# Performance work log

Measured on AMD Instinct MI355X. Metric: run time of the kernel, lower is better.

The kernel has to match this reference:

```python
import jax, jax.numpy as jnp
import numpy as np

EPS = 1e-5

def _layernorm(x, w, b):
    mu = jnp.mean(x, axis=-1, keepdims=True)
    var = jnp.var(x, axis=-1, keepdims=True)
    return (x - mu) * jax.lax.rsqrt(var + EPS) * w + b

def setup_inputs() -> dict:
    key = jax.random.key(0)
    ks = jax.random.split(key, 7)
    b, n, m, d, h = 4, 1024, 1024, 1024, 16
    sc = 1.0 / np.sqrt(d)
    return {
        "x": jax.random.normal(ks[0], (b, n, d), jnp.float32),
        "xa": jax.random.normal(ks[1], (b, m, d), jnp.float32),
        "ln_w": jnp.ones((d,), jnp.float32),
        "ln_b": jnp.zeros((d,), jnp.float32),
        "Wq": jax.random.normal(ks[2], (d, d), jnp.float32) * sc,
        "Wkv": jax.random.normal(ks[3], (d, 2 * d), jnp.float32) * sc,
        "Wout": jax.random.normal(ks[4], (d, d), jnp.float32) * sc,
    }

def reference(x, xa, ln_w, ln_b, Wq, Wkv, Wout):
    b, n, d = x.shape
    m = xa.shape[1]
    h = 16
    hd = d // h

    xn = _layernorm(x, ln_w, ln_b)
    xan = _layernorm(xa, ln_w, ln_b)

    q = xn @ Wq                      # [b,n,d]
    kv = xn @ Wkv                    # [b,n,2d] (k,v unused for x->xa path except v)
    k, v = kv[..., :d], kv[..., d:]
    kva = xan @ Wkv
    ka, va = kva[..., :d], kva[..., d:]

    split = lambda t: t.reshape(t.shape[0], t.shape[1], h, hd).transpose(0, 2, 1, 3)  # [b,h,s,hd]
    q, v, ka, va = map(split, (q, v, ka, va))

    # shared score matrix: scores[b,h,n,m] = q . ka  (no scaling in source)
    scores = jnp.einsum('bhnd,bhmd->bhnm', q, ka)
    # x -> attends over xa: softmax over m
    probs_x = jax.nn.softmax(scores, axis=-1)
    x_upd = jnp.einsum('bhnm,bhmd->bhnd', probs_x, va)
    # xa -> attends over x: softmax over n (of transposed scores)
    probs_xa = jax.nn.softmax(scores.transpose(0, 1, 3, 2), axis=-1)  # [b,h,m,n]
    xa_upd = jnp.einsum('bhmn,bhnd->bhmd', probs_xa, v)

    merge = lambda t: t.transpose(0, 2, 1, 3).reshape(t.shape[0], t.shape[2], d)
    return (merge(x_upd) @ Wout, merge(xa_upd) @ Wout)
```

## Files before the change

### kernel.cpp

```cpp
#include <hip/hip_runtime.h>
#include <hip/hip_bf16.h>

typedef unsigned short u16;
typedef unsigned int u32;
typedef __attribute__((ext_vector_type(4))) unsigned short u16x4;
typedef __attribute__((ext_vector_type(8))) unsigned short u16x8;
typedef __attribute__((ext_vector_type(8))) __bf16 bf16x8;
typedef __attribute__((ext_vector_type(4))) float f32x4;

__device__ __forceinline__ u16 f2bf(float f){
  unsigned u = __builtin_bit_cast(unsigned, f);
  u += 0x7FFFu + ((u >> 16) & 1u);
  return (u16)(u >> 16);
}

__device__ __forceinline__ u32 cvtpk(float lo, float hi){
  u32 r;
  asm("v_cvt_pk_bf16_f32 %0, %1, %2" : "=v"(r) : "v"(lo), "v"(hi));
  return r;
}

__device__ __forceinline__ void load_lds16(const void* g, void* l){
  __builtin_amdgcn_global_load_lds((const __attribute__((address_space(1))) unsigned*)g,
                                   (__attribute__((address_space(3))) unsigned*)l, 16, 0, 0);
}

__device__ __forceinline__ void storeC(float* p, float v){ *p = v; }
__device__ __forceinline__ void storeC(u16* p, float v){ *p = f2bf(v); }

__global__ __launch_bounds__(256) void transpose_all(const float* __restrict__ Wq,
                                                     const float* __restrict__ Wkv,
                                                     const float* __restrict__ Wout,
                                                     u16* __restrict__ WqT, u16* __restrict__ WkT,
                                                     u16* __restrict__ WvT, u16* __restrict__ WoT){
  const float* in; u16* out; int ldin;
  switch (blockIdx.z){
    case 0:  in = Wq;         out = WqT; ldin = 1024; break;
    case 1:  in = Wkv;        out = WkT; ldin = 2048; break;
    case 2:  in = Wkv + 1024; out = WvT; ldin = 2048; break;
    default: in = Wout;       out = WoT; ldin = 1024; break;
  }
  float scl = (blockIdx.z == 0) ? 1.44269504f : 1.0f;
  __shared__ float tile[64][65];
  int t = threadIdx.x;
  int tr = blockIdx.y * 64, tc = blockIdx.x * 64;
  int r0 = t >> 4, c0 = (t & 15) * 4;
#pragma unroll
  for (int i = 0; i < 4; ++i){
    int r = r0 + i * 16;
    const float4 val = *(const float4*)&in[(size_t)(tr + r) * ldin + tc + c0];
    tile[r][c0] = val.x; tile[r][c0+1] = val.y; tile[r][c0+2] = val.z; tile[r][c0+3] = val.w;
  }
  __syncthreads();
#pragma unroll
  for (int i = 0; i < 4; ++i){
    int n = r0 + i * 16;
    u16x4 o4;
    o4.x = f2bf(tile[c0+0][n] * scl); o4.y = f2bf(tile[c0+1][n] * scl);
    o4.z = f2bf(tile[c0+2][n] * scl); o4.w = f2bf(tile[c0+3][n] * scl);
    *(u16x4*)&out[(size_t)(tc + n) * 1024 + tr + c0] = o4;
  }
}

__global__ __launch_bounds__(256) void ln_cast(const float* __restrict__ x, const float* __restrict__ xa,
                                               const float* __restrict__ w, const float* __restrict__ bb,
                                               u16* __restrict__ xn, u16* __restrict__ xan){
  int row = blockIdx.x;
  const float* src; u16* dst;
  if (row < 4096){ src = x + (size_t)row * 1024; dst = xn + (size_t)row * 1024; }
  else { src = xa + (size_t)(row - 4096) * 1024; dst = xan + (size_t)(row - 4096) * 1024; }
  int t = threadIdx.x;
  float4 v = ((const float4*)src)[t];
  float s = v.x + v.y + v.z + v.w;
  float ss = v.x*v.x + v.y*v.y + v.z*v.z + v.w*v.w;
#pragma unroll
  for (int o = 32; o > 0; o >>= 1){ s += __shfl_down(s, o); ss += __shfl_down(ss, o); }
  __shared__ float red[8];
  int wv = t >> 6;
  if ((t & 63) == 0){ red[wv] = s; red[wv + 4] = ss; }
  __syncthreads();
  if (t == 0){
    red[0] = red[0] + red[1] + red[2] + red[3];
    red[4] = red[4] + red[5] + red[6] + red[7];
  }
  __syncthreads();
  float mu = red[0] * (1.0f/1024.0f);
  float var = red[4] * (1.0f/1024.0f) - mu*mu;
  float rstd = rsqrtf(var + 1e-5f);
  float4 wv4 = ((const float4*)w)[t];
  float4 bv4 = ((const float4*)bb)[t];
  u16x4 o4;
  o4.x = f2bf((v.x - mu) * rstd * wv4.x + bv4.x);
  o4.y = f2bf((v.y - mu) * rstd * wv4.y + bv4.y);
  o4.z = f2bf((v.z - mu) * rstd * wv4.z + bv4.z);
  o4.w = f2bf((v.w - mu) * rstd * wv4.w + bv4.w);
  ((u16x4*)dst)[t] = o4;
}

template<int BM, int NQ, int TMASK, typename OutT>
__global__ __launch_bounds__(512, 2) void gemm256(
    const u16* __restrict__ A0, const u16* __restrict__ A1,
    const u16* __restrict__ A2, const u16* __restrict__ A3,
    const u16* __restrict__ B0, const u16* __restrict__ B1,
    const u16* __restrict__ B2, const u16* __restrict__ B3,
    OutT* __restrict__ C0, OutT* __restrict__ C1,
    OutT* __restrict__ C2, OutT* __restrict__ C3){
  constexpr int AI = BM / 64;
  constexpr int FI = BM / 32;
  constexpr int MT = (NQ == 4) ? 16 : 64;
  __shared__ u16 SA[2][BM * 64];
  __shared__ u16 SB[2][16384];
  int tid = threadIdx.x, lane = tid & 63, wave = tid >> 6;
  int g = lane >> 4, r15 = lane & 15;
  int id = blockIdx.x;
  int r8 = id & 7, k = id >> 3;
  int gm = (k >> 2) * 8 + r8;
  int ntile = k & 3;
  int quad = gm / MT;
  int mbase = (gm % MT) * BM, nbase = ntile * 256;
  const u16* A = quad==0?A0:quad==1?A1:quad==2?A2:A3;
  const u16* B = quad==0?B0:quad==1?B1:quad==2?B2:B3;
  OutT* C      = quad==0?C0:quad==1?C1:quad==2?C2:C3;
  int wr = wave >> 2, wc = wave & 3;
  int rsub = lane >> 3;
  int slo  = (lane & 7) ^ ((lane >> 3) & 7);
  int sw8  = (r15 & 7) << 3;
  f32x4 acc[FI][4] = {};

#define STG(kt, b) { \
  int ko = (kt) * 64; \
  _Pragma("unroll") \
  for (int i = 0; i < AI; ++i){ \
    int row = i*64 + wave*8 + rsub; \
    load_lds16(A + (size_t)(mbase + row)*1024 + ko + slo*8, &SA[b][(i*512 + wave*64)*8]); \
  } \
  _Pragma("unroll") \
  for (int i = 0; i < 4; ++i){ \
    int row = i*64 + wave*8 + rsub; \
    load_lds16(B + (size_t)(nbase + row)*1024 + ko + slo*8, &SB[b][(i*512 + wave*64)*8]); \
  } }

  STG(0, 0);
  for (int t = 0; t < 16; ++t){
    int b = t & 1;
    if (t < 15){
      STG(t + 1, b ^ 1);
      if constexpr (AI == 4) asm volatile("s_waitcnt vmcnt(8)" ::: "memory");
      else                   asm volatile("s_waitcnt vmcnt(6)" ::: "memory");
    } else {
      asm volatile("s_waitcnt vmcnt(0)" ::: "memory");
    }
    __builtin_amdgcn_s_barrier();
    __builtin_amdgcn_sched_barrier(0);
    const u16* Al = &SA[b][0];
    const u16* Bl = &SB[b][0];
#pragma unroll
    for (int ks = 0; ks < 2; ++ks){
      bf16x8 af[FI], bfr[4];
#pragma unroll
      for (int fi = 0; fi < FI; ++fi)
        af[fi] = *(const bf16x8*)&Al[(wr*(FI*16) + fi*16 + r15)*64 + ((ks*32 + g*8) ^ sw8)];
#pragma unroll
      for (int fj = 0; fj < 4; ++fj)
        bfr[fj] = *(const bf16x8*)&Bl[(wc*64 + fj*16 + r15)*64 + ((ks*32 + g*8) ^ sw8)];
#pragma unroll
      for (int fi = 0; fi < FI; ++fi)
#pragma unroll
        for (int fj = 0; fj < 4; ++fj)
          acc[fi][fj] = __builtin_amdgcn_mfma_f32_16x16x32_bf16(af[fi], bfr[fj], acc[fi][fj], 0, 0, 0);
    }
    __builtin_amdgcn_s_barrier();
  }
#undef STG

  bool tr = (TMASK >> quad) & 1;
#pragma unroll
  for (int fi = 0; fi < FI; ++fi)
#pragma unroll
    for (int fj = 0; fj < 4; ++fj)
#pragma unroll
      for (int r = 0; r < 4; ++r){
        int row = mbase + wr*(FI*16) + fi*16 + g*4 + r;
        int col = nbase + wc*64 + fj*16 + r15;
        if constexpr (TMASK != 0){
          if (tr){
            int bb = row >> 10, token = row & 1023;
            int hh = col >> 6,  dd = col & 63;
            storeC(&C[((size_t)((bb << 4) + hh) * 64 + dd) * 1024 + token], acc[fi][fj][r]);
            continue;
          }
        }
        storeC(&C[(size_t)row * 1024 + col], acc[fi][fj][r]);
      }
}

#define SW(row, col) ((row) * 64 + ((col) ^ (((row) & 7) << 3)))

__device__ __forceinline__ void exchP(const f32x4& s0, const f32x4& s1,
                                      const f32x4& s2, const f32x4& s3,
                                      bool gh, bool g0, bf16x8& pf0, bf16x8& pf1){
  u32 pk00 = cvtpk(s0[0], s0[1]), pk01 = cvtpk(s0[2], s0[3]);
  u32 pk10 = cvtpk(s1[0], s1[1]), pk11 = cvtpk(s1[2], s1[3]);
  u32 pk20 = cvtpk(s2[0], s2[1]), pk21 = cvtpk(s2[2], s2[3]);
  u32 pk30 = cvtpk(s3[0], s3[1]), pk31 = cvtpk(s3[2], s3[3]);
  u32 c0 = gh ? pk10 : pk00, c1 = gh ? pk11 : pk01;
  u32 d0 = gh ? pk00 : pk10, d1 = gh ? pk01 : pk11;
  u32 s1a = __shfl_xor((int)c0, 16), s1b = __shfl_xor((int)c1, 16);
  u32 s2a = __shfl_xor((int)d0, 32), s2b = __shfl_xor((int)d1, 32);
  u32 s3a = __shfl_xor((int)d0, 48), s3b = __shfl_xor((int)d1, 48);
  union UB { u32 w[4]; bf16x8 v; } ub0, ub1;
  ub0.w[0] = gh ? (g0 ? s1a : s2a) : (g0 ? s3a : c0);
  ub0.w[1] = gh ? (g0 ? s1b : s2b) : (g0 ? s3b : c1);
  ub0.w[2] = gh ? (g0 ? c0 : s3a) : (g0 ? s2a : s1a);
  ub0.w[3] = gh ? (g0 ? c1 : s3b) : (g0 ? s2b : s1b);
  u32 e0 = gh ? pk30 : pk20, e1 = gh ? pk31 : pk21;
  u32 f0 = gh ? pk20 : pk30, f1 = gh ? pk21 : pk31;
  u32 t1a = __shfl_xor((int)e0, 16), t1b = __shfl_xor((int)e1, 16);
  u32 t2a = __shfl_xor((int)f0, 32), t2b = __shfl_xor((int)f1, 32);
  u32 t3a = __shfl_xor((int)f0, 48), t3b = __shfl_xor((int)f1, 48);
  ub1.w[0] = gh ? (g0 ? t1a : t2a) : (g0 ? t3a : e0);
  ub1.w[1] = gh ? (g0 ? t1b : t2b) : (g0 ? t3b : e1);
  ub1.w[2] = gh ? (g0 ? e0 : t3a) : (g0 ? t2a : t1a);
  ub1.w[3] = gh ? (g0 ? e1 : t3b) : (g0 ? t2b : t1b);
  pf0 = ub0.v; pf1 = ub1.v;
}

#define MFMA16(a, b, c) __builtin_amdgcn_mfma_f32_16x16x32_bf16(a, b, c, 0, 0, 0)

__global__ __launch_bounds__(256) void flash(const u16* __restrict__ qg, const u16* __restrict__ vTg,
                                             const u16* __restrict__ kag, const u16* __restrict__ vaTg,
                                             u16* __restrict__ xu, u16* __restrict__ xau){
  __shared__ u16 Ks[4096], VTs[4096];
  int tid = threadIdx.x, lane = tid & 63, wave = tid >> 6, g = lane >> 4, r15 = lane & 15;
  int b = blockIdx.x;
  int xcd = b & 7, idx = b >> 3;
  int qt = idx & 15;
  int pair = xcd * 16 + (idx >> 4);
  int bh = pair & 63, dir = pair >> 6;
  size_t tokbase = ((size_t)(bh >> 4)) * 1048576 + (size_t)(bh & 15) * 64;
  size_t vtbase  = (size_t)bh << 16;
  const u16 *Q, *K, *VT; u16* O;
  if (dir == 0){ Q = qg + tokbase;  K = kag + tokbase; VT = vaTg + vtbase; O = xu  + tokbase; }
  else         { Q = kag + tokbase; K = qg  + tokbase; VT = vTg  + vtbase; O = xau + tokbase; }
  Q += (size_t)qt * 64 * 1024;
  O += (size_t)qt * 64 * 1024;

  int wq = wave * 16;
  bf16x8 qf0 = *(const bf16x8*)&Q[(size_t)(wq + r15) * 1024 + g*8];
  bf16x8 qf1 = *(const bf16x8*)&Q[(size_t)(wq + r15) * 1024 + 32 + g*8];

  int srow = tid >> 3, scol = (tid & 7) * 8;
  const u16* Kp  = K  + (size_t)srow * 1024 + scol;
  const u16* VTp = VT + (size_t)srow * 1024 + scol;
  u16x8 kr0 = *(const u16x8*)(Kp);
  u16x8 kr1 = *(const u16x8*)(Kp + (size_t)32 * 1024);
  u16x8 vr0 = *(const u16x8*)(VTp);
  u16x8 vr1 = *(const u16x8*)(VTp + (size_t)32 * 1024);

  float l = 0.0f;
  f32x4 acc[4] = {};
  bool gh = g >= 2, g0 = g & 1;
  const f32x4 zinit = {-32.f, -32.f, -32.f, -32.f};

  for (int j = 0; j < 16; ++j){
    __syncthreads();
    *(u16x8*)&Ks [SW(srow,      scol)] = kr0;
    *(u16x8*)&Ks [SW(srow + 32, scol)] = kr1;
    *(u16x8*)&VTs[SW(srow,      scol)] = vr0;
    *(u16x8*)&VTs[SW(srow + 32, scol)] = vr1;
    if (j < 15){
      const u16* Kn = Kp  + (size_t)(j + 1) * 64 * 1024;
      const u16* Vn = VTp + (j + 1) * 64;
      kr0 = *(const u16x8*)(Kn);
      kr1 = *(const u16x8*)(Kn + (size_t)32 * 1024);
      vr0 = *(const u16x8*)(Vn);
      vr1 = *(const u16x8*)(Vn + (size_t)32 * 1024);
    }
    __syncthreads();

    f32x4 sf[4];
    __builtin_amdgcn_s_setprio(1);
#pragma unroll
    for (int kvi = 0; kvi < 4; ++kvi){
      bf16x8 kf0 = *(const bf16x8*)&Ks[SW(kvi*16 + r15, g*8)];
      bf16x8 kf1 = *(const bf16x8*)&Ks[SW(kvi*16 + r15, 32 + g*8)];
      f32x4 z = MFMA16(kf0, qf0, zinit);
      z = MFMA16(kf1, qf1, z);
      sf[kvi] = z;
    }
    __builtin_amdgcn_s_setprio(0);

    float psum = 0.0f;
#pragma unroll
    for (int kvi = 0; kvi < 4; ++kvi)
#pragma unroll
      for (int r = 0; r < 4; ++r){
        float p = __builtin_amdgcn_exp2f(sf[kvi][r]);
        sf[kvi][r] = p; psum += p;
      }
    psum += __shfl_xor(psum, 16);
    psum += __shfl_xor(psum, 32);
    l += psum;

    bf16x8 pf0, pf1;
    exchP(sf[0], sf[1], sf[2], sf[3], gh, g0, pf0, pf1);

    __builtin_amdgcn_s_setprio(1);
#pragma unroll
    for (int nb = 0; nb < 4; ++nb){
      bf16x8 vf0 = *(const bf16x8*)&VTs[SW(nb*16 + r15, g*8)];
      acc[nb] = MFMA16(vf0, pf0, acc[nb]);
    }
#pragma unroll
    for (int nb = 0; nb < 4; ++nb){
      bf16x8 vf1 = *(const bf16x8*)&VTs[SW(nb*16 + r15, 32 + g*8)];
      acc[nb] = MFMA16(vf1, pf1, acc[nb]);
    }
    __builtin_amdgcn_s_setprio(0);
  }

  float inv = 1.0f / l;
  size_t orow = (size_t)(wq + r15) * 1024;
#pragma unroll
  for (int nb = 0; nb < 4; ++nb){
    u16x4 o;
    o.x = f2bf(acc[nb][0] * inv);
    o.y = f2bf(acc[nb][1] * inv);
    o.z = f2bf(acc[nb][2] * inv);
    o.w = f2bf(acc[nb][3] * inv);
    *(u16x4*)&O[orow + nb*16 + g*4] = o;
  }
}

extern "C" void kernel_launch(void* const* d_in, const int* in_sizes, int n_in,
                              void* d_out, int out_size, void* d_ws, size_t ws_size,
                              hipStream_t stream){
  const float* x    = (const float*)d_in[0];
  const float* xa   = (const float*)d_in[1];
  const float* lnw  = (const float*)d_in[2];
  const float* lnb  = (const float*)d_in[3];
  const float* Wq   = (const float*)d_in[4];
  const float* Wkv  = (const float*)d_in[5];
  const float* Wout = (const float*)d_in[6];
  float* out = (float*)d_out;
  char* ws = (char*)d_ws;
  const size_t MB = 1ull << 20;
  u16* xn  = (u16*)(ws);
  u16* xan = (u16*)(ws + 8*MB);
  u16* q   = (u16*)(ws + 16*MB);
  u16* vT  = (u16*)(ws + 24*MB);
  u16* ka  = (u16*)(ws + 32*MB);
  u16* vaT = (u16*)(ws + 40*MB);
  u16* xu  = (u16*)(ws + 48*MB);
  u16* xau = (u16*)(ws + 56*MB);
  u16* WqT = (u16*)(ws + 64*MB);
  u16* WkT = (u16*)(ws + 66*MB);
  u16* WvT = (u16*)(ws + 68*MB);
  u16* WoT = (u16*)(ws + 70*MB);
  dim3 blk(256);
  transpose_all<<<dim3(16,16,4), blk, 0, stream>>>(Wq, Wkv, Wout, WqT, WkT, WvT, WoT);
  ln_cast<<<8192, blk, 0, stream>>>(x, xa, lnw, lnb, xn, xan);
  gemm256<256, 4, 0xA, u16><<<dim3(256), dim3(512), 0, stream>>>(
      xn, xn, xan, xan, WqT, WvT, WkT, WvT, q, vT, ka, vaT);
  flash<<<dim3(2048), blk, 0, stream>>>(q, vT, ka, vaT, xu, xau);
  gemm256<128, 1, 0, float><<<dim3(256), dim3(512), 0, stream>>>(
      xu, xu, xu, xu, WoT, WoT, WoT, WoT, out, out, out, out);
}
```

Baseline: 166.1 us.

## Double-buffer flash K/V tiles with direct global-to-LDS async loads

Replaces the register-staged K/V tile loads with global_load_lds async copies into a double-buffered shared memory region. The next tile is prefetched while the current one is consumed, with vmcnt waits and raw barriers in place of the two __syncthreads per iteration. It also defers the cross-lane row-sum shuffle reduction to after the loop. LDS usage doubles, and the swizzle now relies on the XOR chunk mapping in the load addresses matching the SW() layout, which is hard to confirm from the shown code.

New measurement: 164.0 us (median of 2 runs). Within noise of the previous version (-1.3%).

```diff
diff --git a/kernel.cpp b/kernel.cpp
--- a/kernel.cpp
+++ b/kernel.cpp
@@ -230,7 +230,7 @@
 __global__ __launch_bounds__(256) void flash(const u16* __restrict__ qg, const u16* __restrict__ vTg,
                                              const u16* __restrict__ kag, const u16* __restrict__ vaTg,
                                              u16* __restrict__ xu, u16* __restrict__ xau){
-  __shared__ u16 Ks[4096], VTs[4096];
+  __shared__ u16 Ks[2][4096], VTs[2][4096];
   int tid = threadIdx.x, lane = tid & 63, wave = tid >> 6, g = lane >> 4, r15 = lane & 15;
   int b = blockIdx.x;
   int xcd = b & 7, idx = b >> 3;
@@ -249,58 +249,56 @@
   bf16x8 qf0 = *(const bf16x8*)&Q[(size_t)(wq + r15) * 1024 + g*8];
   bf16x8 qf1 = *(const bf16x8*)&Q[(size_t)(wq + r15) * 1024 + 32 + g*8];
 
-  int srow = tid >> 3, scol = (tid & 7) * 8;
-  const u16* Kp  = K  + (size_t)srow * 1024 + scol;
-  const u16* VTp = VT + (size_t)srow * 1024 + scol;
-  u16x8 kr0 = *(const u16x8*)(Kp);
-  u16x8 kr1 = *(const u16x8*)(Kp + (size_t)32 * 1024);
-  u16x8 vr0 = *(const u16x8*)(VTp);
-  u16x8 vr1 = *(const u16x8*)(VTp + (size_t)32 * 1024);
-
-  float l = 0.0f;
+  int rl = lane >> 3;
+  int ch = (lane & 7) ^ rl;
+  const u16* Kb = K  + (size_t)(wave*8 + rl) * 1024 + ch*8;
+  const u16* Vb = VT + (size_t)(wave*8 + rl) * 1024 + ch*8;
+
+#define FSTG(j, buf) { \
+  load_lds16(Kb + (size_t)(j)*65536,                 &Ks [buf][(wave*8)*64]); \
+  load_lds16(Kb + (size_t)(j)*65536 + 32*1024,       &Ks [buf][(wave*8 + 32)*64]); \
+  load_lds16(Vb + (j)*64,                            &VTs[buf][(wave*8)*64]); \
+  load_lds16(Vb + (j)*64 + (size_t)32*1024,          &VTs[buf][(wave*8 + 32)*64]); \
+}
+
+  float pl = 0.0f;
   f32x4 acc[4] = {};
   bool gh = g >= 2, g0 = g & 1;
   const f32x4 zinit = {-32.f, -32.f, -32.f, -32.f};
 
+  FSTG(0, 0);
   for (int j = 0; j < 16; ++j){
-    __syncthreads();
-    *(u16x8*)&Ks [SW(srow,      scol)] = kr0;
-    *(u16x8*)&Ks [SW(srow + 32, scol)] = kr1;
-    *(u16x8*)&VTs[SW(srow,      scol)] = vr0;
-    *(u16x8*)&VTs[SW(srow + 32, scol)] = vr1;
+    int buf = j & 1;
     if (j < 15){
-      const u16* Kn = Kp  + (size_t)(j + 1) * 64 * 1024;
-      const u16* Vn = VTp + (j + 1) * 64;
-      kr0 = *(const u16x8*)(Kn);
-      kr1 = *(const u16x8*)(Kn + (size_t)32 * 1024);
-      vr0 = *(const u16x8*)(Vn);
-      vr1 = *(const u16x8*)(Vn + (size_t)32 * 1024);
-    }
-    __syncthreads();
+      FSTG(j + 1, buf ^ 1);
+      asm volatile("s_waitcnt vmcnt(4)" ::: "memory");
+    } else {
+      asm volatile("s_waitcnt vmcnt(0)" ::: "memory");
+    }
+    __builtin_amdgcn_s_barrier();
+    __builtin_amdgcn_sched_barrier(0);
+    const u16* kb = &Ks[buf][0];
+    const u16* vb = &VTs[buf][0];
 
     f32x4 sf[4];
     __builtin_amdgcn_s_setprio(1);
 #pragma unroll
     for (int kvi = 0; kvi < 4; ++kvi){
-      bf16x8 kf0 = *(const bf16x8*)&Ks[SW(kvi*16 + r15, g*8)];
-      bf16x8 kf1 = *(const bf16x8*)&Ks[SW(kvi*16 + r15, 32 + g*8)];
+      bf16x8 kf0 = *(const bf16x8*)&kb[SW(kvi*16 + r15, g*8)];
+      bf16x8 kf1 = *(const bf16x8*)&kb[SW(kvi*16 + r15, 32 + g*8)];
       f32x4 z = MFMA16(kf0, qf0, zinit);
       z = MFMA16(kf1, qf1, z);
       sf[kvi] = z;
     }
     __builtin_amdgcn_s_setprio(0);
 
-    float psum = 0.0f;
 #pragma unroll
     for (int kvi = 0; kvi < 4; ++kvi)
 #pragma unroll
       for (int r = 0; r < 4; ++r){
         float p = __builtin_amdgcn_exp2f(sf[kvi][r]);
-        sf[kvi][r] = p; psum += p;
+        sf[kvi][r] = p; pl += p;
       }
-    psum += __shfl_xor(psum, 16);
-    psum += __shfl_xor(psum, 32);
-    l += psum;
 
     bf16x8 pf0, pf1;
     exchP(sf[0], sf[1], sf[2], sf[3], gh, g0, pf0, pf1);
@@ -308,18 +306,22 @@
     __builtin_amdgcn_s_setprio(1);
 #pragma unroll
     for (int nb = 0; nb < 4; ++nb){
-      bf16x8 vf0 = *(const bf16x8*)&VTs[SW(nb*16 + r15, g*8)];
+      bf16x8 vf0 = *(const bf16x8*)&vb[SW(nb*16 + r15, g*8)];
       acc[nb] = MFMA16(vf0, pf0, acc[nb]);
     }
 #pragma unroll
     for (int nb = 0; nb < 4; ++nb){
-      bf16x8 vf1 = *(const bf16x8*)&VTs[SW(nb*16 + r15, 32 + g*8)];
+      bf16x8 vf1 = *(const bf16x8*)&vb[SW(nb*16 + r15, 32 + g*8)];
       acc[nb] = MFMA16(vf1, pf1, acc[nb]);
     }
     __builtin_amdgcn_s_setprio(0);
-  }
-
-  float inv = 1.0f / l;
+    __builtin_amdgcn_s_barrier();
+  }
+#undef FSTG
+
+  pl += __shfl_xor(pl, 16);
+  pl += __shfl_xor(pl, 32);
+  float inv = 1.0f / pl;
   size_t orow = (size_t)(wq + r15) * 1024;
 #pragma unroll
   for (int nb = 0; nb < 4; ++nb){
```

## Replace QKV projection GEMM with 8-phase software-pipelined LDS GEMM kernel

Applied to the files above, without the earlier changes.

Adds a new gemm8p kernel for the fused Q/V/Ka/Va projection. It splits each K-tile into two half-K LDS buffers, interleaves the next tile's global-to-LDS loads with MFMA phases, uses partial vmcnt waits and s_setprio around the MFMA bursts, and remaps the block index for XCD locality. The aim is to hide global load latency behind matrix math. In exchange it brings many barriers per iteration and larger LDS use (128 KB per block), which limits occupancy.

Result: no change. 165.1 us (-0.6%).

```diff
diff --git a/kernel.cpp b/kernel.cpp
--- a/kernel.cpp
+++ b/kernel.cpp
@@ -7,6 +7,8 @@
 typedef __attribute__((ext_vector_type(8))) unsigned short u16x8;
 typedef __attribute__((ext_vector_type(8))) __bf16 bf16x8;
 typedef __attribute__((ext_vector_type(4))) float f32x4;
+
+#define MFMA16(a, b, c) __builtin_amdgcn_mfma_f32_16x16x32_bf16(a, b, c, 0, 0, 0)
 
 __device__ __forceinline__ u16 f2bf(float f){
   unsigned u = __builtin_bit_cast(unsigned, f);
@@ -167,7 +169,7 @@
       for (int fi = 0; fi < FI; ++fi)
 #pragma unroll
         for (int fj = 0; fj < 4; ++fj)
-          acc[fi][fj] = __builtin_amdgcn_mfma_f32_16x16x32_bf16(af[fi], bfr[fj], acc[fi][fj], 0, 0, 0);
+          acc[fi][fj] = MFMA16(af[fi], bfr[fj], acc[fi][fj]);
     }
     __builtin_amdgcn_s_barrier();
   }
@@ -191,6 +193,114 @@
           }
         }
         storeC(&C[(size_t)row * 1024 + col], acc[fi][fj][r]);
+      }
+}
+
+template<int TMASK>
+__global__ __launch_bounds__(512, 2) void gemm8p(
+    const u16* __restrict__ A0, const u16* __restrict__ A1,
+    const u16* __restrict__ A2, const u16* __restrict__ A3,
+    const u16* __restrict__ B0, const u16* __restrict__ B1,
+    const u16* __restrict__ B2, const u16* __restrict__ B3,
+    u16* __restrict__ C0, u16* __restrict__ C1,
+    u16* __restrict__ C2, u16* __restrict__ C3){
+  __shared__ u16 SL[2][2][2][8192];
+  int tid = threadIdx.x, lane = tid & 63, wave = tid >> 6;
+  int g = lane >> 4, r15 = lane & 15;
+  int id = blockIdx.x;
+  int r8 = id & 7, k = id >> 3;
+  int gm = (k >> 2) * 8 + r8;
+  int ntile = k & 3;
+  int quad = gm >> 4;
+  int mbase = (gm & 15) * 256, nbase = ntile * 256;
+  const u16* A = quad==0?A0:quad==1?A1:quad==2?A2:A3;
+  const u16* B = quad==0?B0:quad==1?B1:quad==2?B2:B3;
+  u16* C       = quad==0?C0:quad==1?C1:quad==2?C2:C3;
+  int wr = wave >> 2, wc = wave & 3;
+  int X = (r15 & 3) ^ ((r15 >> 2) & 3);
+  int rdc = (g ^ X) * 8;
+  int srA = wave * 16 + (lane >> 2);
+  int csrc = ((lane & 3) ^ ((lane >> 2) & 3) ^ ((lane >> 4) & 3)) * 8;
+  f32x4 acc[8][4] = {};
+  bf16x8 af[4], bfr[4];
+
+#define ST8(P, tb, kt, kh, m, db) { \
+  load_lds16(P + (size_t)((tb) + srA)*1024 + (kt)*64 + (kh)*32 + csrc,       &SL[m][db][kh][wave*512]); \
+  load_lds16(P + (size_t)((tb) + 128 + srA)*1024 + (kt)*64 + (kh)*32 + csrc, &SL[m][db][kh][4096 + wave*512]); }
+
+#define RD_A(db, kh, bfi) { \
+  _Pragma("unroll") \
+  for (int q = 0; q < 4; ++q) \
+    af[q] = *(const bf16x8*)&SL[0][db][kh][(wr*128 + ((bfi)+q)*16 + r15)*32 + rdc]; }
+
+#define RD_B(db, kh) { \
+  _Pragma("unroll") \
+  for (int q = 0; q < 4; ++q) \
+    bfr[q] = *(const bf16x8*)&SL[1][db][kh][(wc*64 + q*16 + r15)*32 + rdc]; }
+
+#define MM8(bfi) { \
+  _Pragma("unroll") \
+  for (int q = 0; q < 4; ++q) \
+    _Pragma("unroll") \
+    for (int fj = 0; fj < 4; ++fj) \
+      acc[(bfi)+q][fj] = MFMA16(af[q], bfr[fj], acc[(bfi)+q][fj]); }
+
+#define PH(db, kh, half, STAGE, WAIT) { \
+  if ((half) == 0) RD_B(db, kh); \
+  RD_A(db, kh, (half)*4); \
+  STAGE; \
+  WAIT; \
+  __builtin_amdgcn_s_barrier(); \
+  asm volatile("s_waitcnt lgkmcnt(0)" ::: "memory"); \
+  __builtin_amdgcn_sched_barrier(0); \
+  __builtin_amdgcn_s_setprio(1); \
+  MM8((half)*4); \
+  __builtin_amdgcn_s_setprio(0); \
+  __builtin_amdgcn_s_barrier(); }
+
+  ST8(A, mbase, 0, 0, 0, 0); ST8(B, nbase, 0, 0, 1, 0);
+  ST8(A, mbase, 0, 1, 0, 0); ST8(B, nbase, 0, 1, 1, 0);
+  ST8(A, mbase, 1, 0, 0, 1); ST8(B, nbase, 1, 0, 1, 1);
+  asm volatile("s_waitcnt vmcnt(4)" ::: "memory");
+  __builtin_amdgcn_s_barrier();
+
+  for (int i = 0; i < 8; ++i){
+    int t1 = 2*i + 1, t2 = 2*i + 2, t3 = 2*i + 3;
+    bool more = (i < 7);
+    PH(0, 0, 0, ST8(A, mbase, t1, 1, 0, 1), {});
+    PH(0, 0, 1, ST8(B, nbase, t1, 1, 1, 1), {});
+    PH(0, 1, 0, { if (more) ST8(A, mbase, t2, 0, 0, 0); }, {});
+    PH(0, 1, 1, { if (more) ST8(B, nbase, t2, 0, 1, 0); },
+                { if (more) asm volatile("s_waitcnt vmcnt(4)" ::: "memory");
+                  else      asm volatile("s_waitcnt vmcnt(0)" ::: "memory"); });
+    PH(1, 0, 0, { if (more) ST8(A, mbase, t2, 1, 0, 0); }, {});
+    PH(1, 0, 1, { if (more) ST8(B, nbase, t2, 1, 1, 0); }, {});
+    PH(1, 1, 0, { if (more) ST8(A, mbase, t3, 0, 0, 1); }, {});
+    PH(1, 1, 1, { if (more) ST8(B, nbase, t3, 0, 1, 1); },
+                { if (more) asm volatile("s_waitcnt vmcnt(4)" ::: "memory"); });
+  }
+#undef PH
+#undef MM8
+#undef RD_B
+#undef RD_A
+#undef ST8
+
+  bool tr = (TMASK >> quad) & 1;
+#pragma unroll
+  for (int fi = 0; fi < 8; ++fi)
+#pragma unroll
+    for (int fj = 0; fj < 4; ++fj)
+#pragma unroll
+      for (int r = 0; r < 4; ++r){
+        int row = mbase + wr*128 + fi*16 + g*4 + r;
+        int col = nbase + wc*64 + fj*16 + r15;
+        if (tr){
+          int bb = row >> 10, token = row & 1023;
+          int hh = col >> 6,  dd = col & 63;
+          storeC(&C[((size_t)((bb << 4) + hh) * 64 + dd) * 1024 + token], acc[fi][fj][r]);
+        } else {
+          storeC(&C[(size_t)row * 1024 + col], acc[fi][fj][r]);
+        }
       }
 }
 
@@ -224,8 +334,6 @@
   ub1.w[3] = gh ? (g0 ? e1 : t3b) : (g0 ? t2b : t1b);
   pf0 = ub0.v; pf1 = ub1.v;
 }
-
-#define MFMA16(a, b, c) __builtin_amdgcn_mfma_f32_16x16x32_bf16(a, b, c, 0, 0, 0)
 
 __global__ __launch_bounds__(256) void flash(const u16* __restrict__ qg, const u16* __restrict__ vTg,
                                              const u16* __restrict__ kag, const u16* __restrict__ vaTg,
@@ -360,7 +468,7 @@
   dim3 blk(256);
   transpose_all<<<dim3(16,16,4), blk, 0, stream>>>(Wq, Wkv, Wout, WqT, WkT, WvT, WoT);
   ln_cast<<<8192, blk, 0, stream>>>(x, xa, lnw, lnb, xn, xan);
-  gemm256<256, 4, 0xA, u16><<<dim3(256), dim3(512), 0, stream>>>(
+  gemm8p<0xA><<<dim3(256), dim3(512), 0, stream>>>(
       xn, xn, xan, xan, WqT, WvT, WkT, WvT, q, vT, ka, vaT);
   flash<<<dim3(2048), blk, 0, stream>>>(q, vT, ka, vaT, xu, xau);
   gemm256<128, 1, 0, float><<<dim3(256), dim3(512), 0, stream>>>(
```
